# Kernel tuning notes

Measured on AMD Instinct MI355X. Metric: run time of the kernel, lower is better.

The kernel has to match this reference:

```python
import jax, jax.numpy as jnp
import numpy as np

N_ENT, N_REL, D, H, K, B = 100000, 100, 128, 2, 64, 8192


def _xavier(key, shape):
    fan_in, fan_out = shape[-1], shape[-2] if len(shape) >= 2 else shape[-1]
    a = (6.0 / (fan_in + fan_out)) ** 0.5
    return jax.random.uniform(key, shape, jnp.float32, -a, a)


def setup_inputs() -> dict:
    key = jax.random.key(0)
    ks = jax.random.split(key, 16)
    inp = {
        'u1': jax.random.randint(ks[0], (B,), 0, N_ENT, jnp.int32),
        'u2': jax.random.randint(ks[1], (B,), 0, N_ENT, jnp.int32),
        'c': jax.random.randint(ks[2], (B,), 0, N_ENT, jnp.int32),
        'adj_entity': jax.random.randint(ks[3], (N_ENT, K), 0, N_ENT, jnp.int32),
        'adj_relation': jax.random.randint(ks[4], (N_ENT, K), 0, N_REL, jnp.int32),
        # learned parameters (torch Linear convention: weight [out, in])
        'entity_emb': _xavier(ks[5], (N_ENT, D)),
        'relation_emb': _xavier(ks[6], (N_REL, D)),
        'Wa1': _xavier(ks[7], (D, 2 * D)),
        'Wa2': _xavier(ks[8], (D, D)),
        'Wa3': _xavier(ks[9], (1, D)),
        # per-head Wx (original code creates a fresh nn.Linear(dim,dim) inside the
        # head loop each call; we materialize it as a deterministic per-head param)
        'Wx': _xavier(ks[10], (H, D, D)),
        'bx': jax.random.uniform(ks[11], (H, D), jnp.float32, -1, 1) / np.sqrt(D),
        'W1': _xavier(ks[12], (2 * D, H * D)),
        'b1': jax.random.uniform(ks[13], (2 * D,), jnp.float32, -1, 1) / np.sqrt(H * D),
        'W2': _xavier(ks[14], (2 * D, H * D)),
        'b2': jax.random.uniform(ks[15], (2 * D,), jnp.float32, -1, 1) / np.sqrt(H * D),
    }
    return inp


def _lookup(table, idx):
    # nn.Embedding(max_norm=1): rows with norm > 1 are renormalized to norm 1
    v = table[idx]
    n = jnp.sqrt(jnp.sum(v * v, axis=-1, keepdims=True))
    return v * jnp.where(n > 1.0, 1.0 / (n + 1e-7), 1.0)


def _leaky(x):
    return jax.nn.leaky_relu(x, 0.2)


def _branch(e_idx, entity_emb, relation_emb, Wa1, Wa2, Wa3, Wx, bx, W1, b1, W2, b2,
            adj_entity, adj_relation):
    t_idx = adj_entity[e_idx]          # [B, K]
    r_idx = adj_relation[e_idx]        # [B, K]
    h = _lookup(entity_emb, e_idx)     # [B, D]
    t = _lookup(entity_emb, t_idx)     # [B, K, D]
    r = _lookup(relation_emb, r_idx)   # [B, K, D]
    hb = jnp.broadcast_to(h[:, None, :], t.shape)
    x = jnp.concatenate([hb, r], axis=-1)                 # [B, K, 2D]
    a = jax.nn.relu(jnp.einsum('bkf,df->bkd', x, Wa1))
    a = jax.nn.relu(jnp.einsum('bkd,ed->bke', a, Wa2))
    a = jax.nn.sigmoid(jnp.einsum('bkd,od->bko', a, Wa3))[..., 0]  # [B, K]
    w = jax.nn.softmax(a, axis=-1)
    s = jnp.einsum('bk,bkd->bd', w, t)                    # weighted sum of tails
    # per-head output projection (attention weights are head-independent)
    heads = jnp.einsum('bd,hed->bhe', s, Wx) + bx         # [B, H, D]
    vec = _leaky(heads.reshape(heads.shape[0], -1))       # [B, H*D]
    hrep = jnp.tile(h, (1, Wx.shape[0]))                  # [B, H*D]
    agg = _leaky((hrep + vec) @ W1.T + b1) + _leaky((hrep * vec) @ W2.T + b2)  # [B, 2D]
    # sum_aggregator(agg='concat'): cat(embs[1], embs[0])
    return jnp.concatenate([agg, h], axis=-1)             # [B, 3D]


def reference(u1, u2, c, adj_entity, adj_relation, entity_emb, relation_emb,
              Wa1, Wa2, Wa3, Wx, bx, W1, b1, W2, b2):
    params = (entity_emb, relation_emb, Wa1, Wa2, Wa3, Wx, bx, W1, b1, W2, b2)
    cell = _branch(c, *params, adj_entity, adj_relation)
    d2 = _branch(u2, *params, adj_entity, adj_relation)
    d1 = _branch(u1, *params, adj_entity, adj_relation)
    combine = jnp.maximum(d1, d2)
    return jax.nn.sigmoid(jnp.sum(combine * cell, axis=1))
```

## Files before the change

kernel.cpp:

```cpp
#include <hip/hip_runtime.h>
#include <hip/hip_bf16.h>
#include <cstdint>
#include <cstddef>

#define NENT 100000
#define NREL 100
#define DD   128
#define KK   64
#define BB   8192

typedef __bf16 bf16x8 __attribute__((ext_vector_type(8)));
typedef float  f32x4  __attribute__((ext_vector_type(4)));
typedef unsigned int u32x4 __attribute__((ext_vector_type(4)));

__device__ __forceinline__ unsigned short f2bf(float x) {
    union { float f; unsigned u; } v; v.f = x;
    unsigned r = v.u + 0x7fffu + ((v.u >> 16) & 1u);
    return (unsigned short)(r >> 16);
}
__device__ __forceinline__ float bf2f(unsigned short h) {
    union { unsigned u; float f; } v; v.u = ((unsigned)h) << 16;
    return v.f;
}
__device__ __forceinline__ float leakyf(float x) { return x >= 0.f ? x : 0.2f * x; }
__device__ __forceinline__ float sigmoidf(float x) { return 1.f / (1.f + __expf(-x)); }
__device__ __forceinline__ f32x4 mfma16(bf16x8 a, bf16x8 b, f32x4 c) {
    return __builtin_amdgcn_mfma_f32_16x16x32_bf16(a, b, c, 0, 0, 0);
}


__global__ __launch_bounds__(256) void prep_emb(const float* __restrict__ src,
                                                unsigned short* __restrict__ dst,
                                                int rows) {
    const int lane = threadIdx.x & 63;
    const int row  = blockIdx.x * 4 + (threadIdx.x >> 6);
    if (row >= rows) return;
    const float2 v = *(const float2*)(src + (size_t)row * DD + 2 * lane);
    float sq = v.x * v.x + v.y * v.y;
#pragma unroll
    for (int off = 32; off; off >>= 1) sq += __shfl_xor(sq, off);
    const float n = sqrtf(sq);
    const float s = n > 1.f ? 1.f / (n + 1e-7f) : 1.f;
    unsigned int pk = (unsigned)f2bf(v.x * s) | ((unsigned)f2bf(v.y * s) << 16);
    *(unsigned int*)(dst + (size_t)row * DD + 2 * lane) = pk;
}

__global__ __launch_bounds__(256) void prep_w(
    const float* __restrict__ Wa1, const float* __restrict__ Wa2,
    const float* __restrict__ Wx, const float* __restrict__ W1, const float* __restrict__ W2,
    unsigned short* __restrict__ Wa1b, unsigned short* __restrict__ Wa2b,
    unsigned short* __restrict__ Wxb, unsigned short* __restrict__ W1b,
    unsigned short* __restrict__ W2b) {
    int i = blockIdx.x * 256 + threadIdx.x;
    if (i < 32768)        Wa1b[i]          = f2bf(Wa1[i]);
    else if (i < 49152)   Wa2b[i - 32768]  = f2bf(Wa2[i - 32768]);
    else if (i < 81920)   Wxb[i - 49152]   = f2bf(Wx[i - 49152]);
    else if (i < 147456)  W1b[i - 81920]   = f2bf(W1[i - 81920]);
    else if (i < 212992)  W2b[i - 147456]  = f2bf(W2[i - 147456]);
}

__global__ __launch_bounds__(128) void relp_k(const float* __restrict__ relE,
                                              const float* __restrict__ Wa1f,
                                              unsigned short* __restrict__ relPb) {
    __shared__ float rl[DD];
    __shared__ float red[2];
    const int r = blockIdx.x, d = threadIdx.x, lane = d & 63, wv = d >> 6;
    const float v = relE[(size_t)r * DD + d];
    float sq = v * v;
#pragma unroll
    for (int off = 32; off; off >>= 1) sq += __shfl_xor(sq, off);
    if (lane == 0) red[wv] = sq;
    __syncthreads();
    const float n = sqrtf(red[0] + red[1]);
    const float scl = n > 1.f ? 1.f / (n + 1e-7f) : 1.f;
    rl[d] = v * scl;
    __syncthreads();
    float acc = 0.f;
#pragma unroll 4
    for (int j = 0; j < DD; ++j) acc += rl[j] * Wa1f[(size_t)d * 256 + DD + j];
    relPb[(size_t)r * DD + d] = f2bf(acc);
}

__global__ __launch_bounds__(256) void hh_gemm(
    const int* __restrict__ u1, const int* __restrict__ u2, const int* __restrict__ cI,
    const unsigned short* __restrict__ entB,
    const unsigned short* __restrict__ Wa1b,
    float* __restrict__ HHo) {
    constexpr int AS = 136;
    __shared__ __align__(16) unsigned short AL[64 * AS];
    __shared__ int eL[64];
    const int t = threadIdx.x, lane = t & 63, w = t >> 6, g = lane >> 4, li = lane & 15;
    const int m0 = blockIdx.x * 64;
    const int branch = m0 >> 13, b0 = m0 & (BB - 1);
    const int* ep = branch == 0 ? u1 : branch == 1 ? u2 : cI;
    if (t < 64) eL[t] = ep[b0 + t];
    __syncthreads();
    for (int idx = t; idx < 4096; idx += 256) {
        const int row = idx >> 6, cc = idx & 63;
        *(unsigned int*)&AL[row * AS + cc * 2] =
            ((const unsigned int*)(entB + (size_t)eL[row] * DD))[cc];
    }
    __syncthreads();
    f32x4 acc[4][2] = {};
#pragma unroll
    for (int ks = 0; ks < 4; ++ks) {
        const int kb = ks * 32 + g * 8;
        const bf16x8 bw0 = *(const bf16x8*)(Wa1b + (size_t)((w * 2 + 0) * 16 + li) * 256 + kb);
        const bf16x8 bw1 = *(const bf16x8*)(Wa1b + (size_t)((w * 2 + 1) * 16 + li) * 256 + kb);
#pragma unroll
        for (int mt = 0; mt < 4; ++mt) {
            const bf16x8 a = *(const bf16x8*)(&AL[(mt * 16 + li) * AS + kb]);
            acc[mt][0] = mfma16(a, bw0, acc[mt][0]);
            acc[mt][1] = mfma16(a, bw1, acc[mt][1]);
        }
    }
#pragma unroll
    for (int mt = 0; mt < 4; ++mt)
#pragma unroll
        for (int ntl = 0; ntl < 2; ++ntl) {
            const int col = (w * 2 + ntl) * 16 + li;
#pragma unroll
            for (int i = 0; i < 4; ++i) {
                const int row = mt * 16 + g * 4 + i;
                HHo[(size_t)(m0 + row) * DD + col] = acc[mt][ntl][i];
            }
        }
}


__global__ __launch_bounds__(512, 4) void attn_tail(
    const int* __restrict__ u1, const int* __restrict__ u2, const int* __restrict__ cI,
    const int* __restrict__ adj_e, const int* __restrict__ adj_r,
    const unsigned short* __restrict__ entB,
    const unsigned short* __restrict__ relPb,
    const unsigned short* __restrict__ Wa2b,
    const float* __restrict__ Wa3,
    const float* __restrict__ HHp,
    unsigned short* __restrict__ s_bf) {
    __shared__ __align__(16) unsigned short WL[DD * DD];

    const int t = threadIdx.x;
    const int lane = t & 63, w = t >> 6;
    const int g = lane >> 4, li = lane & 15;

    {
        const unsigned int* src = (const unsigned int*)Wa2b;
        unsigned int* dst = (unsigned int*)WL;
#pragma unroll
        for (int it = 0; it < 16; ++it) {
            const int i = t + it * 512;
            const int d = i >> 6, c2 = i & 63;
            const int B = c2 >> 2, j2 = c2 & 3;
            dst[d * 64 + (((B ^ (d & 15))) << 2) + j2] = src[i];
        }
    }

    const int s = blockIdx.x * 8 + w;
    const int branch = s >> 13, b = s & (BB - 1);
    const int e = (branch == 0 ? u1 : branch == 1 ? u2 : cI)[b];
    const int tIr = adj_e[(size_t)e * KK + lane];
    const int rIr = adj_r[(size_t)e * KK + lane];

    int rr4[4];
#pragma unroll
    for (int bt = 0; bt < 4; ++bt) rr4[bt] = __shfl(rIr, bt * 16 + li);

    f32x4 he[4], ho[4];
#pragma unroll
    for (int ks = 0; ks < 4; ++ks) {
        const float* p = HHp + (size_t)s * DD + ks * 32 + g * 8;
        const f32x4 a = *(const f32x4*)p;
        const f32x4 bq = *(const f32x4*)(p + 4);
        he[ks] = (f32x4){a[0], a[2], bq[0], bq[2]};
        ho[ks] = (f32x4){a[1], a[3], bq[1], bq[3]};
    }

    bf16x8 afr[4][4];
#pragma unroll
    for (int bt = 0; bt < 4; ++bt) {
        const unsigned short* pr = relPb + ((size_t)rr4[bt] << 7) + (g << 3);
#pragma unroll
        for (int ks = 0; ks < 4; ++ks) {
            const u32x4 pw = *(const u32x4*)(pr + (ks << 5));
            f32x4 pe, po;
#pragma unroll
            for (int j = 0; j < 4; ++j) {
                pe[j] = __uint_as_float(pw[j] << 16);
                po[j] = __uint_as_float(pw[j] & 0xffff0000u);
            }
            pe += he[ks];
            po += ho[ks];
#pragma unroll
            for (int j = 0; j < 4; ++j) {
                afr[bt][ks][2 * j]     = (__bf16)fmaxf(pe[j], 0.f);
                afr[bt][ks][2 * j + 1] = (__bf16)fmaxf(po[j], 0.f);
            }
        }
    }

    __syncthreads();

    f32x4 pd2 = {};
    const int wrow = li << 7;
#pragma unroll
    for (int nt = 0; nt < 8; ++nt) {
        bf16x8 bfr[4];
#pragma unroll
        for (int ks = 0; ks < 4; ++ks)
            bfr[ks] = *(const bf16x8*)(&WL[(nt << 11) + wrow + (((ks * 4 + g) ^ li) << 3)]);
        const f32x4 w3f = *(const f32x4*)(Wa3 + nt * 16 + g * 4);
        f32x4 acc[4] = {};
#pragma unroll
        for (int ks = 0; ks < 4; ++ks)
#pragma unroll
            for (int bt = 0; bt < 4; ++bt) acc[bt] = mfma16(bfr[ks], afr[bt][ks], acc[bt]);
#pragma unroll
        for (int bt = 0; bt < 4; ++bt) {
            pd2[bt] += fmaxf(acc[bt][0], 0.f) * w3f[0] + fmaxf(acc[bt][1], 0.f) * w3f[1] +
                       fmaxf(acc[bt][2], 0.f) * w3f[2] + fmaxf(acc[bt][3], 0.f) * w3f[3];
        }
    }

    bf16x8 tv[16];
#pragma unroll
    for (int mt = 0; mt < 4; ++mt)
#pragma unroll
        for (int i = 0; i < 4; ++i) {
            const int r = mt * 16 + g * 4 + i;
            const int ti = __shfl(tIr, r);
            tv[mt * 4 + i] = *(const bf16x8*)(entB + (size_t)ti * DD + li * 8);
        }

#pragma unroll
    for (int bt = 0; bt < 4; ++bt) {
        pd2[bt] += __shfl_xor(pd2[bt], 16);
        pd2[bt] += __shfl_xor(pd2[bt], 32);
    }

    float avn[4];
    float sm = 0.f;
#pragma unroll
    for (int bt = 0; bt < 4; ++bt) {
        avn[bt] = __expf(sigmoidf(pd2[bt]));
        sm += avn[bt];
    }
#pragma unroll
    for (int off = 1; off < 16; off <<= 1) sm += __shfl_xor(sm, off);
    const float inv = 1.f / sm;
    float ws4[4];
#pragma unroll
    for (int bt = 0; bt < 4; ++bt) ws4[bt] = avn[bt] * inv;

    float s8[8] = {0.f};
#pragma unroll
    for (int mt = 0; mt < 4; ++mt)
#pragma unroll
        for (int i = 0; i < 4; ++i) {
            const float wt = __shfl(ws4[mt], g * 4 + i);
            const bf16x8 t8 = tv[mt * 4 + i];
#pragma unroll
            for (int j = 0; j < 8; ++j) s8[j] += wt * (float)t8[j];
        }
#pragma unroll
    for (int j = 0; j < 8; ++j) {
        s8[j] += __shfl_xor(s8[j], 16);
        s8[j] += __shfl_xor(s8[j], 32);
    }
    if (lane < 16) {
        union { bf16x8 v; unsigned short u[8]; } sv;
#pragma unroll
        for (int j = 0; j < 8; ++j) sv.u[j] = f2bf(s8[j]);
        *(bf16x8*)(s_bf + (size_t)s * DD + li * 8) = sv.v;
    }
}


__global__ __launch_bounds__(256, 3) void head_agg2(
    const int* __restrict__ u1, const int* __restrict__ u2, const int* __restrict__ cI,
    const unsigned short* __restrict__ s_bf, const unsigned short* __restrict__ entB,
    const unsigned short* __restrict__ Wxb, const float* __restrict__ bx,
    const unsigned short* __restrict__ W1b, const float* __restrict__ b1,
    const unsigned short* __restrict__ W2b, const float* __restrict__ b2,
    float* __restrict__ agg_ws) {
    constexpr int SBS = 136, HS = 132, YS = 264;
    __shared__ __align__(16) unsigned short SB[32 * SBS];
    __shared__ __align__(16) unsigned short HLb[32 * HS];
    __shared__ __align__(16) unsigned short Y1[32 * YS];
    __shared__ __align__(16) unsigned short Y2[32 * YS];
    __shared__ unsigned short bxl[256], b1l[256], b2l[256];
    __shared__ int eL[32];

    const int t = threadIdx.x;
    const int lane = t & 63, w = t >> 6;
    const int g = lane >> 4, li = lane & 15;
    const int r = blockIdx.x >> 8;
    const int m0 = (blockIdx.x & 255) * 32;
    const size_t base = (size_t)r * BB + m0;
    const int* ep = r == 0 ? u1 : r == 1 ? u2 : cI;

    if (t < 32) eL[t] = ep[m0 + t];
    bxl[t] = f2bf(bx[t]); b1l[t] = f2bf(b1[t]); b2l[t] = f2bf(b2[t]);
    __syncthreads();

    for (int idx = t; idx < 2048; idx += 256) {
        const int row = idx >> 6, cc = idx & 63;
        *(unsigned int*)&SB[row * SBS + cc * 2] =
            ((const unsigned int*)(s_bf + (base + row) * DD))[cc];
        *(unsigned int*)&HLb[row * HS + cc * 2] =
            ((const unsigned int*)(entB + (size_t)eL[row] * DD))[cc];
    }
    __syncthreads();

    f32x4 ah[2][4] = {};
#pragma unroll
    for (int ks = 0; ks < 4; ++ks) {
        const int kb = ks * 32 + g * 8;
        bf16x8 bb[4];
#pragma unroll
        for (int ntl = 0; ntl < 4; ++ntl)
            bb[ntl] = *(const bf16x8*)(Wxb + ((size_t)(w * 4 + ntl) * 16 + li) * DD + kb);
#pragma unroll
        for (int mt = 0; mt < 2; ++mt) {
            const bf16x8 a = *(const bf16x8*)(&SB[(mt * 16 + li) * SBS + kb]);
#pragma unroll
            for (int ntl = 0; ntl < 4; ++ntl) ah[mt][ntl] = mfma16(a, bb[ntl], ah[mt][ntl]);
        }
    }
#pragma unroll
    for (int mt = 0; mt < 2; ++mt)
#pragma unroll
        for (int ntl = 0; ntl < 4; ++ntl) {
            const int col = (w * 4 + ntl) * 16 + li;
            const int ee = col & 127;
#pragma unroll
            for (int i = 0; i < 4; ++i) {
                const int row = mt * 16 + g * 4 + i;
                const float v = ah[mt][ntl][i] + bf2f(bxl[col]);
                const float vec = leakyf(v);
                const float hvv = bf2f(HLb[row * HS + ee]);
                Y1[row * YS + col] = f2bf(hvv + vec);
                Y2[row * YS + col] = f2bf(hvv * vec);
            }
        }
    __syncthreads();

    f32x4 ac1[2][4] = {}, ac2[2][4] = {};
#pragma unroll
    for (int ks = 0; ks < 8; ++ks) {
        const int kb = ks * 32 + g * 8;
        bf16x8 bb1[4], bb2[4];
#pragma unroll
        for (int ntl = 0; ntl < 4; ++ntl) {
            bb1[ntl] = *(const bf16x8*)(W1b + ((size_t)(w * 4 + ntl) * 16 + li) * 256 + kb);
            bb2[ntl] = *(const bf16x8*)(W2b + ((size_t)(w * 4 + ntl) * 16 + li) * 256 + kb);
        }
#pragma unroll
        for (int mt = 0; mt < 2; ++mt) {
            const bf16x8 a1 = *(const bf16x8*)(&Y1[(mt * 16 + li) * YS + kb]);
            const bf16x8 a2 = *(const bf16x8*)(&Y2[(mt * 16 + li) * YS + kb]);
#pragma unroll
            for (int ntl = 0; ntl < 4; ++ntl) {
                ac1[mt][ntl] = mfma16(a1, bb1[ntl], ac1[mt][ntl]);
                ac2[mt][ntl] = mfma16(a2, bb2[ntl], ac2[mt][ntl]);
            }
        }
    }
#pragma unroll
    for (int mt = 0; mt < 2; ++mt)
#pragma unroll
        for (int ntl = 0; ntl < 4; ++ntl) {
            const int col = (w * 4 + ntl) * 16 + li;
#pragma unroll
            for (int i = 0; i < 4; ++i) {
                const int row = mt * 16 + g * 4 + i;
                const float x1 = leakyf(ac1[mt][ntl][i] + bf2f(b1l[col]));
                const float x2 = leakyf(ac2[mt][ntl][i] + bf2f(b2l[col]));
                agg_ws[(base + row) * 256 + col] = x1 + x2;
            }
        }
}


__global__ __launch_bounds__(256) void final_dot2(
    const int* __restrict__ u1, const int* __restrict__ u2, const int* __restrict__ cI,
    const float* __restrict__ agg_ws, const unsigned short* __restrict__ entB,
    float* __restrict__ out) {
    const int t = threadIdx.x;
    const int lane = t & 63, w = t >> 6;
    const int b = blockIdx.x * 4 + w;
    const float* a1p = agg_ws + (size_t)b * 256;
    const float* a2p = agg_ws + ((size_t)BB + b) * 256;
    const float* acp = agg_ws + ((size_t)2 * BB + b) * 256;
    float acc = 0.f;
#pragma unroll
    for (int j = lane; j < 256; j += 64) acc += fmaxf(a1p[j], a2p[j]) * acp[j];
    const unsigned short* h1p = entB + (size_t)u1[b] * DD;
    const unsigned short* h2p = entB + (size_t)u2[b] * DD;
    const unsigned short* hcp = entB + (size_t)cI[b] * DD;
#pragma unroll
    for (int j = lane; j < DD; j += 64)
        acc += fmaxf(bf2f(h1p[j]), bf2f(h2p[j])) * bf2f(hcp[j]);
#pragma unroll
    for (int off = 32; off; off >>= 1) acc += __shfl_down(acc, off);
    if (lane == 0) out[b] = sigmoidf(acc);
}


extern "C" void kernel_launch(void* const* d_in, const int* in_sizes, int n_in,
                              void* d_out, int out_size, void* d_ws, size_t ws_size,
                              hipStream_t stream) {
    (void)in_sizes; (void)n_in; (void)out_size; (void)ws_size;
    const int*   u1   = (const int*)d_in[0];
    const int*   u2   = (const int*)d_in[1];
    const int*   cI   = (const int*)d_in[2];
    const int*   adjE = (const int*)d_in[3];
    const int*   adjR = (const int*)d_in[4];
    const float* entE = (const float*)d_in[5];
    const float* relE = (const float*)d_in[6];
    const float* Wa1  = (const float*)d_in[7];
    const float* Wa2  = (const float*)d_in[8];
    const float* Wa3  = (const float*)d_in[9];
    const float* Wx   = (const float*)d_in[10];
    const float* bx   = (const float*)d_in[11];
    const float* W1   = (const float*)d_in[12];
    const float* b1   = (const float*)d_in[13];
    const float* W2   = (const float*)d_in[14];
    const float* b2   = (const float*)d_in[15];
    float* out = (float*)d_out;

    char* ws = (char*)d_ws;
    unsigned short* entB = (unsigned short*)(ws);
    unsigned short* Wa1b = (unsigned short*)(ws + 25600000);
    unsigned short* Wa2b = (unsigned short*)(ws + 25665536);
    unsigned short* Wxb  = (unsigned short*)(ws + 25698304);
    unsigned short* W1b  = (unsigned short*)(ws + 25763840);
    unsigned short* W2b  = (unsigned short*)(ws + 25894912);
    unsigned short* relPb = (unsigned short*)(ws + 26025984);
    float* HHp   = (float*)(ws + 26051584);
    unsigned short* s_bf = (unsigned short*)(ws + 44925952);
    float* agg_ws = (float*)(ws + 51217408);

    hipLaunchKernelGGL(prep_emb, dim3(NENT / 4), dim3(256), 0, stream, entE, entB, NENT);
    hipLaunchKernelGGL(prep_w, dim3(832), dim3(256), 0, stream, Wa1, Wa2, Wx, W1, W2,
                       Wa1b, Wa2b, Wxb, W1b, W2b);
    hipLaunchKernelGGL(relp_k, dim3(NREL), dim3(128), 0, stream, relE, Wa1, relPb);
    hipLaunchKernelGGL(hh_gemm, dim3(3 * BB / 64), dim3(256), 0, stream,
                       u1, u2, cI, entB, Wa1b, HHp);
    hipLaunchKernelGGL(attn_tail, dim3(3 * BB / 8), dim3(512), 0, stream,
                       u1, u2, cI, adjE, adjR, entB, relPb, Wa2b, Wa3, HHp, s_bf);
    hipLaunchKernelGGL(head_agg2, dim3(3 * (BB / 32)), dim3(256), 0, stream,
                       u1, u2, cI, s_bf, entB, Wxb, bx, W1b, b1, W2b, b2, agg_ws);
    hipLaunchKernelGGL(final_dot2, dim3(BB / 4), dim3(256), 0, stream,
                       u1, u2, cI, agg_ws, entB, out);
}
```

Baseline: 189.2 us.

## Fuse head aggregation with final max-dot-sigmoid, grouping three branches per block

Each block of the head aggregation kernel now handles 16 batch rows across all three branches (48 rows total) instead of 32 rows of a single branch. This lets it compute the max/product/sum and sigmoid in-register and write the final output directly. The separate final_dot2 kernel and the fp32 agg workspace round-trip (3×8192×256 floats written then re-read) are removed. In exchange the block uses more shared memory, more accumulator registers, a lower occupancy hint, and half as many rows per branch per block, so weight loads are amortized over fewer rows.

```diff
diff --git a/kernel.cpp b/kernel.cpp
--- a/kernel.cpp
+++ b/kernel.cpp
@@ -275,43 +275,46 @@
 }
 
 
-__global__ __launch_bounds__(256, 3) void head_agg2(
+__global__ __launch_bounds__(256, 2) void head_agg3(
     const int* __restrict__ u1, const int* __restrict__ u2, const int* __restrict__ cI,
     const unsigned short* __restrict__ s_bf, const unsigned short* __restrict__ entB,
     const unsigned short* __restrict__ Wxb, const float* __restrict__ bx,
     const unsigned short* __restrict__ W1b, const float* __restrict__ b1,
     const unsigned short* __restrict__ W2b, const float* __restrict__ b2,
-    float* __restrict__ agg_ws) {
+    float* __restrict__ out) {
     constexpr int SBS = 136, HS = 132, YS = 264;
-    __shared__ __align__(16) unsigned short SB[32 * SBS];
-    __shared__ __align__(16) unsigned short HLb[32 * HS];
-    __shared__ __align__(16) unsigned short Y1[32 * YS];
-    __shared__ __align__(16) unsigned short Y2[32 * YS];
+    __shared__ __align__(16) unsigned short SB[48 * SBS];
+    __shared__ __align__(16) unsigned short HLb[48 * HS];
+    __shared__ __align__(16) unsigned short Y1[48 * YS];
+    __shared__ __align__(16) unsigned short Y2[48 * YS];
     __shared__ unsigned short bxl[256], b1l[256], b2l[256];
-    __shared__ int eL[32];
+    __shared__ int eL[48];
+    __shared__ float prr[4][16];
 
     const int t = threadIdx.x;
     const int lane = t & 63, w = t >> 6;
     const int g = lane >> 4, li = lane & 15;
-    const int r = blockIdx.x >> 8;
-    const int m0 = (blockIdx.x & 255) * 32;
-    const size_t base = (size_t)r * BB + m0;
-    const int* ep = r == 0 ? u1 : r == 1 ? u2 : cI;
-
-    if (t < 32) eL[t] = ep[m0 + t];
+    const int m0 = blockIdx.x * 16;
+
+    if (t < 48) {
+        const int br = t >> 4, j = t & 15;
+        eL[t] = (br == 0 ? u1 : br == 1 ? u2 : cI)[m0 + j];
+    }
     bxl[t] = f2bf(bx[t]); b1l[t] = f2bf(b1[t]); b2l[t] = f2bf(b2[t]);
     __syncthreads();
 
-    for (int idx = t; idx < 2048; idx += 256) {
+    for (int idx = t; idx < 3072; idx += 256) {
         const int row = idx >> 6, cc = idx & 63;
+        const int br = row >> 4, j = row & 15;
+        const size_t sidx = (size_t)br * BB + m0 + j;
         *(unsigned int*)&SB[row * SBS + cc * 2] =
-            ((const unsigned int*)(s_bf + (base + row) * DD))[cc];
+            ((const unsigned int*)(s_bf + sidx * DD))[cc];
         *(unsigned int*)&HLb[row * HS + cc * 2] =
             ((const unsigned int*)(entB + (size_t)eL[row] * DD))[cc];
     }
     __syncthreads();
 
-    f32x4 ah[2][4] = {};
+    f32x4 ah[3][4] = {};
 #pragma unroll
     for (int ks = 0; ks < 4; ++ks) {
         const int kb = ks * 32 + g * 8;
@@ -320,14 +323,14 @@
         for (int ntl = 0; ntl < 4; ++ntl)
             bb[ntl] = *(const bf16x8*)(Wxb + ((size_t)(w * 4 + ntl) * 16 + li) * DD + kb);
 #pragma unroll
-        for (int mt = 0; mt < 2; ++mt) {
+        for (int mt = 0; mt < 3; ++mt) {
             const bf16x8 a = *(const bf16x8*)(&SB[(mt * 16 + li) * SBS + kb]);
 #pragma unroll
             for (int ntl = 0; ntl < 4; ++ntl) ah[mt][ntl] = mfma16(a, bb[ntl], ah[mt][ntl]);
         }
     }
 #pragma unroll
-    for (int mt = 0; mt < 2; ++mt)
+    for (int mt = 0; mt < 3; ++mt)
 #pragma unroll
         for (int ntl = 0; ntl < 4; ++ntl) {
             const int col = (w * 4 + ntl) * 16 + li;
@@ -344,7 +347,7 @@
         }
     __syncthreads();
 
-    f32x4 ac1[2][4] = {}, ac2[2][4] = {};
+    f32x4 ac1[3][4] = {}, ac2[3][4] = {};
 #pragma unroll
     for (int ks = 0; ks < 8; ++ks) {
         const int kb = ks * 32 + g * 8;
@@ -355,7 +358,7 @@
             bb2[ntl] = *(const bf16x8*)(W2b + ((size_t)(w * 4 + ntl) * 16 + li) * 256 + kb);
         }
 #pragma unroll
-        for (int mt = 0; mt < 2; ++mt) {
+        for (int mt = 0; mt < 3; ++mt) {
             const bf16x8 a1 = *(const bf16x8*)(&Y1[(mt * 16 + li) * YS + kb]);
             const bf16x8 a2 = *(const bf16x8*)(&Y2[(mt * 16 + li) * YS + kb]);
 #pragma unroll
@@ -365,44 +368,46 @@
             }
         }
     }
-#pragma unroll
-    for (int mt = 0; mt < 2; ++mt)
-#pragma unroll
-        for (int ntl = 0; ntl < 4; ++ntl) {
-            const int col = (w * 4 + ntl) * 16 + li;
-#pragma unroll
-            for (int i = 0; i < 4; ++i) {
-                const int row = mt * 16 + g * 4 + i;
-                const float x1 = leakyf(ac1[mt][ntl][i] + bf2f(b1l[col]));
-                const float x2 = leakyf(ac2[mt][ntl][i] + bf2f(b2l[col]));
-                agg_ws[(base + row) * 256 + col] = x1 + x2;
-            }
-        }
-}
-
-
-__global__ __launch_bounds__(256) void final_dot2(
-    const int* __restrict__ u1, const int* __restrict__ u2, const int* __restrict__ cI,
-    const float* __restrict__ agg_ws, const unsigned short* __restrict__ entB,
-    float* __restrict__ out) {
-    const int t = threadIdx.x;
-    const int lane = t & 63, w = t >> 6;
-    const int b = blockIdx.x * 4 + w;
-    const float* a1p = agg_ws + (size_t)b * 256;
-    const float* a2p = agg_ws + ((size_t)BB + b) * 256;
-    const float* acp = agg_ws + ((size_t)2 * BB + b) * 256;
-    float acc = 0.f;
-#pragma unroll
-    for (int j = lane; j < 256; j += 64) acc += fmaxf(a1p[j], a2p[j]) * acp[j];
-    const unsigned short* h1p = entB + (size_t)u1[b] * DD;
-    const unsigned short* h2p = entB + (size_t)u2[b] * DD;
-    const unsigned short* hcp = entB + (size_t)cI[b] * DD;
-#pragma unroll
-    for (int j = lane; j < DD; j += 64)
-        acc += fmaxf(bf2f(h1p[j]), bf2f(h2p[j])) * bf2f(hcp[j]);
-#pragma unroll
-    for (int off = 32; off; off >>= 1) acc += __shfl_down(acc, off);
-    if (lane == 0) out[b] = sigmoidf(acc);
+
+    float part[4] = {0.f, 0.f, 0.f, 0.f};
+#pragma unroll
+    for (int ntl = 0; ntl < 4; ++ntl) {
+        const int col = (w * 4 + ntl) * 16 + li;
+        const float bb1v = bf2f(b1l[col]), bb2v = bf2f(b2l[col]);
+#pragma unroll
+        for (int i = 0; i < 4; ++i) {
+            const float x0 = leakyf(ac1[0][ntl][i] + bb1v) + leakyf(ac2[0][ntl][i] + bb2v);
+            const float x1 = leakyf(ac1[1][ntl][i] + bb1v) + leakyf(ac2[1][ntl][i] + bb2v);
+            const float x2 = leakyf(ac1[2][ntl][i] + bb1v) + leakyf(ac2[2][ntl][i] + bb2v);
+            part[i] += fmaxf(x0, x1) * x2;
+        }
+    }
+#pragma unroll
+    for (int off = 1; off < 16; off <<= 1)
+#pragma unroll
+        for (int i = 0; i < 4; ++i) part[i] += __shfl_xor(part[i], off);
+    if (li == 0) {
+#pragma unroll
+        for (int i = 0; i < 4; ++i) prr[w][g * 4 + i] = part[i];
+    }
+    __syncthreads();
+
+    {
+        const int j = t >> 4, dl = (t & 15) * 8;
+        const unsigned short* h1p = &HLb[(0 * 16 + j) * HS + dl];
+        const unsigned short* h2p = &HLb[(1 * 16 + j) * HS + dl];
+        const unsigned short* hcp = &HLb[(2 * 16 + j) * HS + dl];
+        float a = 0.f;
+#pragma unroll
+        for (int jj = 0; jj < 8; ++jj)
+            a += fmaxf(bf2f(h1p[jj]), bf2f(h2p[jj])) * bf2f(hcp[jj]);
+#pragma unroll
+        for (int off = 1; off < 16; off <<= 1) a += __shfl_xor(a, off);
+        if ((t & 15) == 0) {
+            const float tot = prr[0][j] + prr[1][j] + prr[2][j] + prr[3][j] + a;
+            out[m0 + j] = sigmoidf(tot);
+        }
+    }
 }
 
 
@@ -438,7 +443,6 @@
     unsigned short* relPb = (unsigned short*)(ws + 26025984);
     float* HHp   = (float*)(ws + 26051584);
     unsigned short* s_bf = (unsigned short*)(ws + 44925952);
-    float* agg_ws = (float*)(ws + 51217408);
 
     hipLaunchKernelGGL(prep_emb, dim3(NENT / 4), dim3(256), 0, stream, entE, entB, NENT);
     hipLaunchKernelGGL(prep_w, dim3(832), dim3(256), 0, stream, Wa1, Wa2, Wx, W1, W2,
@@ -448,8 +452,6 @@
                        u1, u2, cI, entB, Wa1b, HHp);
     hipLaunchKernelGGL(attn_tail, dim3(3 * BB / 8), dim3(512), 0, stream,
                        u1, u2, cI, adjE, adjR, entB, relPb, Wa2b, Wa3, HHp, s_bf);
-    hipLaunchKernelGGL(head_agg2, dim3(3 * (BB / 32)), dim3(256), 0, stream,
-                       u1, u2, cI, s_bf, entB, Wxb, bx, W1b, b1, W2b, b2, agg_ws);
-    hipLaunchKernelGGL(final_dot2, dim3(BB / 4), dim3(256), 0, stream,
-                       u1, u2, cI, agg_ws, entB, out);
-}
+    hipLaunchKernelGGL(head_agg3, dim3(BB / 16), dim3(256), 0, stream,
+                       u1, u2, cI, s_bf, entB, Wxb, bx, W1b, b1, W2b, b2, out);
+}
```

Result: faster. 176.7 us (median of 2 runs) (-6.6%).
